# Performance work log

Hardware: AMD Instinct MI355X
Metric: run time of the kernel (lower is better)

## Reference

```python
import jax, jax.numpy as jnp
import numpy as np
from jax import ops as jops

N_NODES = 100000
N_EDGES = 1600000
NEG_SLOPE = 0.2
LN_EPS = 1e-5


def setup_inputs() -> dict:
    key = jax.random.key(0)
    ks = jax.random.split(key, 12)
    inp = {
        "x": jax.random.normal(ks[0], (N_NODES, 4), jnp.float32),
        "edge_index": jax.random.randint(ks[1], (2, N_EDGES), 0, N_NODES, jnp.int64 if jax.config.jax_enable_x64 else jnp.int32),
        # layer 1: GATv2Conv(4, 16, heads=4)
        "W1l": jax.random.normal(ks[2], (4, 64), jnp.float32) * 0.5,
        "W1r": jax.random.normal(ks[3], (4, 64), jnp.float32) * 0.5,
        "a1": jax.random.normal(ks[4], (4, 16), jnp.float32) * 0.5,  # [heads, out]
        "b1": jax.random.normal(ks[5], (64,), jnp.float32) * 0.1,
        "g1": jnp.ones((64,), jnp.float32),
        "be1": jnp.zeros((64,), jnp.float32),
        # layer 2: GATv2Conv(64, 32, heads=1)
        "W2l": jax.random.normal(ks[6], (64, 32), jnp.float32) * 0.125,
        "W2r": jax.random.normal(ks[7], (64, 32), jnp.float32) * 0.125,
        "a2": jax.random.normal(ks[8], (1, 32), jnp.float32) * 0.5,
        "b2": jax.random.normal(ks[9], (32,), jnp.float32) * 0.1,
        "g2": jnp.ones((32,), jnp.float32),
        "be2": jnp.zeros((32,), jnp.float32),
    }
    return inp


def _add_self_loops(edge_index, n):
    loop = jnp.arange(n, dtype=edge_index.dtype)
    return jnp.concatenate([edge_index, jnp.stack([loop, loop])], axis=1)


def _gatv2(x, src, dst, Wl, Wr, att, bias, heads, out_ch, n):
    # x: [N, F]; Wl/Wr: [F, heads*out_ch]; att: [heads, out_ch]
    xl = (x @ Wl).reshape(n, heads, out_ch)  # source transform
    xr = (x @ Wr).reshape(n, heads, out_ch)  # target transform
    e = xl[src] + xr[dst]                     # [E, H, C]
    e = jnp.where(e >= 0, e, NEG_SLOPE * e)   # LeakyReLU(0.2)
    logits = jnp.einsum('ehc,hc->eh', e, att)  # [E, H]
    # segment softmax over destination node
    m = jops.segment_max(logits, dst, num_segments=n)  # [N, H]
    ex = jnp.exp(logits - m[dst])
    denom = jops.segment_sum(ex, dst, num_segments=n)  # [N, H]
    alpha = ex / denom[dst]                            # [E, H]
    out = jops.segment_sum(alpha[:, :, None] * xl[src], dst, num_segments=n)  # [N, H, C]
    return out.reshape(n, heads * out_ch) + bias


def _layernorm(x, g, b):
    mu = jnp.mean(x, axis=-1, keepdims=True)
    var = jnp.mean(jnp.square(x - mu), axis=-1, keepdims=True)
    return (x - mu) * jax.lax.rsqrt(var + LN_EPS) * g + b


def reference(x, edge_index, W1l, W1r, a1, b1, g1, be1, W2l, W2r, a2, b2, g2, be2):
    n = x.shape[0]
    ei = _add_self_loops(edge_index, n)
    src, dst = ei[0], ei[1]
    h = _gatv2(x, src, dst, W1l, W1r, a1, b1, heads=4, out_ch=16, n=n)
    h = _layernorm(h, g1, be1)
    h = jnp.where(h > 0, h, jnp.expm1(h))  # ELU
    h = _gatv2(h, src, dst, W2l, W2r, a2, b2, heads=1, out_ch=32, n=n)
    h = _layernorm(h, g2, be2)
    return h
```

## Files before the change

### kernel.cpp

```cpp
#include <hip/hip_runtime.h>
#include <math.h>

#define NN 100000
#define E0 1600000
#define ETOT (E0 + NN)
#define NEG 0.2f

#define NB 512
#define BS 196
#define CHUNK 4096
#define PPT 16
#define MAXP 4096

__device__ __forceinline__ float leaky(float v) { return fmaxf(v, NEG * v); }

__global__ void k_bhist(const int* __restrict__ ei, int* __restrict__ bcnt) {
    __shared__ int h[NB];
    int tid = threadIdx.x;
    for (int i = tid; i < NB; i += 256) h[i] = 0;
    __syncthreads();
    int stride = gridDim.x * 256;
    for (int e = blockIdx.x * 256 + tid; e < E0; e += stride)
        atomicAdd(&h[ei[E0 + e] / BS], 1);
    __syncthreads();
    for (int i = tid; i < NB; i += 256)
        if (h[i]) atomicAdd(&bcnt[i], h[i]);
}

__global__ void k_bscan(const int* __restrict__ bcnt, int* __restrict__ boff,
                        int* __restrict__ srcsBase, int* __restrict__ cursor) {
    __shared__ int s[NB];
    int tid = threadIdx.x;
    int v = bcnt[tid];
    s[tid] = v;
    __syncthreads();
    for (int off = 1; off < NB; off <<= 1) {
        int t = (tid >= off) ? s[tid - off] : 0;
        __syncthreads();
        s[tid] += t;
        __syncthreads();
    }
    int excl = s[tid] - v;
    boff[tid] = excl;
    cursor[tid] = excl;
    int n0 = tid * BS;
    if (n0 > NN) n0 = NN;
    srcsBase[tid] = excl + n0;
}

__global__ void k_bin(const int* __restrict__ ei, int* __restrict__ cursor,
                      int2* __restrict__ binned) {
    __shared__ int hist[NB];
    __shared__ int basesh[NB];
    int tid = threadIdx.x;
    long long cbase = (long long)blockIdx.x * CHUNK;
    for (int i = tid; i < NB; i += 256) hist[i] = 0;
    __syncthreads();
    int srcv[PPT], dstv[PPT], rank[PPT], bkt[PPT];
#pragma unroll
    for (int k = 0; k < PPT; ++k) {
        long long e = cbase + k * 256 + tid;
        if (e < E0) {
            int s_ = ei[e];
            int d_ = ei[E0 + e];
            int b = d_ / BS;
            rank[k] = atomicAdd(&hist[b], 1);
            srcv[k] = s_;
            dstv[k] = d_;
            bkt[k] = b;
        } else {
            bkt[k] = -1;
        }
    }
    __syncthreads();
    for (int i = tid; i < NB; i += 256)
        if (hist[i] > 0) basesh[i] = atomicAdd(&cursor[i], hist[i]);
    __syncthreads();
#pragma unroll
    for (int k = 0; k < PPT; ++k)
        if (bkt[k] >= 0) {
            int2 p;
            p.x = srcv[k];
            p.y = dstv[k];
            binned[basesh[bkt[k]] + rank[k]] = p;
        }
}

__global__ void k_bfin(const int2* __restrict__ binned, const int* __restrict__ bcnt,
                       const int* __restrict__ boff, const int* __restrict__ srcsBase,
                       int* __restrict__ rs, int* __restrict__ srcs) {
    int b = blockIdx.x;
    int n0 = b * BS;
    if (n0 >= NN) return;
    int nd = NN - n0;
    if (nd > BS) nd = BS;
    int cnt = bcnt[b];
    if (cnt > MAXP) cnt = MAXP;
    int base = boff[b];
    int sb = srcsBase[b];
    __shared__ int ldsCnt[256];
    __shared__ int scanA[256];
    __shared__ int rowOffE[256];
    __shared__ int stage[MAXP + BS];
    int tid = threadIdx.x;
    ldsCnt[tid] = 0;
    __syncthreads();
    int srcv[PPT], dl_[PPT], rk_[PPT];
#pragma unroll
    for (int k = 0; k < PPT; ++k) {
        int i = k * 256 + tid;
        if (i < cnt) {
            int2 p = binned[base + i];
            int dl = p.y - n0;
            rk_[k] = atomicAdd(&ldsCnt[dl], 1);
            srcv[k] = p.x;
            dl_[k] = dl;
        } else {
            dl_[k] = -1;
        }
    }
    __syncthreads();
    int v = (tid < nd) ? ldsCnt[tid] + 1 : 0;
    scanA[tid] = v;
    __syncthreads();
    for (int off = 1; off < 256; off <<= 1) {
        int t = (tid >= off) ? scanA[tid - off] : 0;
        __syncthreads();
        scanA[tid] += t;
        __syncthreads();
    }
    rowOffE[tid] = scanA[tid] - v;
    __syncthreads();
    if (tid < nd) {
        int e = rowOffE[tid];
        rs[n0 + tid] = sb + e;
        stage[e] = n0 + tid;
    }
    __syncthreads();
#pragma unroll
    for (int k = 0; k < PPT; ++k)
        if (dl_[k] >= 0) stage[rowOffE[dl_[k]] + 1 + rk_[k]] = srcv[k];
    __syncthreads();
    int tot = cnt + nd;
    for (int i = tid; i < tot; i += 256) srcs[sb + i] = stage[i];
}

__global__ void k_gat1(const float* __restrict__ x, const float* __restrict__ Wl,
                       const float* __restrict__ Wr, const float* __restrict__ att,
                       const int* __restrict__ rs, const int* __restrict__ srcs,
                       const float* __restrict__ b, const float* __restrict__ g,
                       const float* __restrict__ be, float* __restrict__ h) {
    int lane = threadIdx.x & 63;
    int wave = (blockIdx.x * blockDim.x + threadIdx.x) >> 6;
    int nwaves = (gridDim.x * blockDim.x) >> 6;
    int e_i = lane >> 3;
    int sub = lane & 7;
    float wl[4][8], wr[4][8], at[8];
#pragma unroll
    for (int k = 0; k < 4; ++k)
#pragma unroll
        for (int j = 0; j < 8; ++j) {
            wl[k][j] = Wl[k * 64 + sub * 8 + j];
            wr[k][j] = Wr[k * 64 + sub * 8 + j];
        }
#pragma unroll
    for (int j = 0; j < 8; ++j) at[j] = att[sub * 8 + j];

    for (int n = wave; n < NN; n += nwaves) {
        const float4 xd = *(const float4*)(x + (long long)n * 4);
        float xrd[8];
#pragma unroll
        for (int j = 0; j < 8; ++j)
            xrd[j] = xd.x * wr[0][j] + xd.y * wr[1][j] + xd.z * wr[2][j] +
                     xd.w * wr[3][j];
        int beg = rs[n];
        int end = (n == NN - 1) ? ETOT : rs[n + 1];
        float acc[8] = {0.f, 0.f, 0.f, 0.f, 0.f, 0.f, 0.f, 0.f};
        float den = 0.f;
        for (int base = beg; base < end; base += 8) {
            int slot = base + e_i;
            bool valid = slot < end;
            int s = srcs[valid ? slot : beg];
            const float4 xa = *(const float4*)(x + (long long)s * 4);
            float xls[8];
            float p = 0.f;
#pragma unroll
            for (int j = 0; j < 8; ++j) {
                float t = xa.x * wl[0][j] + xa.y * wl[1][j] + xa.z * wl[2][j] +
                          xa.w * wl[3][j];
                xls[j] = t;
                float u = t + xrd[j];
                u = fmaxf(u, NEG * u);
                p += u * at[j];
            }
            p += __shfl_xor(p, 1);
            float ex = valid ? __expf(p) : 0.f;
            den += ex;
#pragma unroll
            for (int j = 0; j < 8; ++j) acc[j] += ex * xls[j];
        }
#pragma unroll
        for (int m = 8; m <= 32; m <<= 1) {
#pragma unroll
            for (int j = 0; j < 8; ++j) acc[j] += __shfl_xor(acc[j], m);
            den += __shfl_xor(den, m);
        }
        float v = acc[0];
#pragma unroll
        for (int j = 1; j < 8; ++j) v = (e_i == j) ? acc[j] : v;
        int cf = sub * 8 + e_i;
        v = v / den + b[cf];
        float s1 = v;
#pragma unroll
        for (int m = 1; m < 64; m <<= 1) s1 += __shfl_xor(s1, m);
        float mu = s1 * (1.f / 64.f);
        float c = v - mu;
        float sq = c * c;
#pragma unroll
        for (int m = 1; m < 64; m <<= 1) sq += __shfl_xor(sq, m);
        float y = c * rsqrtf(sq * (1.f / 64.f) + 1e-5f) * g[cf] + be[cf];
        h[(long long)n * 64 + cf] = y > 0.f ? y : expm1f(y);
    }
}

__global__ void k_lin2(const float* __restrict__ h, const float* __restrict__ Wl,
                       const float* __restrict__ Wr, float* __restrict__ xl2,
                       float* __restrict__ xr2) {
    __shared__ float wl_s[2048];
    __shared__ float wr_s[2048];
    for (int i = threadIdx.x; i < 2048; i += blockDim.x) {
        wl_s[i] = Wl[i];
        wr_s[i] = Wr[i];
    }
    __syncthreads();
    int t = blockIdx.x * blockDim.x + threadIdx.x;
    if (t >= NN * 32) return;
    int n = t >> 5, j = t & 31;
    const float* hr = h + (long long)n * 64;
    float al = 0.f, ar = 0.f;
#pragma unroll 8
    for (int k = 0; k < 64; ++k) {
        float hv = hr[k];
        al += hv * wl_s[k * 32 + j];
        ar += hv * wr_s[k * 32 + j];
    }
    xl2[(long long)n * 32 + j] = al;
    xr2[(long long)n * 32 + j] = ar;
}

__global__ void k_gat2(const float* __restrict__ xl2, const float* __restrict__ xr2,
                       const float* __restrict__ att, const int* __restrict__ rs,
                       const int* __restrict__ srcs, const float* __restrict__ b,
                       const float* __restrict__ g, const float* __restrict__ be,
                       float* __restrict__ out) {
    int lane = threadIdx.x & 63;
    int wave = (blockIdx.x * blockDim.x + threadIdx.x) >> 6;
    int nwaves = (gridDim.x * blockDim.x) >> 6;
    int e_i = lane >> 3;
    int cg = lane & 7;
    float at[4];
#pragma unroll
    for (int j = 0; j < 4; ++j) at[j] = att[cg * 4 + j];

    for (int n = wave; n < NN; n += nwaves) {
        const float4 xr4 = *(const float4*)(xr2 + (long long)n * 32 + cg * 4);
        float xrd[4] = {xr4.x, xr4.y, xr4.z, xr4.w};
        int beg = rs[n];
        int end = (n == NN - 1) ? ETOT : rs[n + 1];
        float acc[4] = {0.f, 0.f, 0.f, 0.f};
        float den = 0.f;
        for (int base = beg; base < end; base += 8) {
            int slot = base + e_i;
            bool valid = slot < end;
            int s = srcs[valid ? slot : beg];
            const float4 xa = *(const float4*)(xl2 + (long long)s * 32 + cg * 4);
            float xls[4] = {xa.x, xa.y, xa.z, xa.w};
            float p = 0.f;
#pragma unroll
            for (int j = 0; j < 4; ++j) {
                float u = xls[j] + xrd[j];
                u = fmaxf(u, NEG * u);
                p += u * at[j];
            }
            p += __shfl_xor(p, 1);
            p += __shfl_xor(p, 2);
            p += __shfl_xor(p, 4);
            float ex = valid ? __expf(p) : 0.f;
            den += ex;
#pragma unroll
            for (int j = 0; j < 4; ++j) acc[j] += ex * xls[j];
        }
#pragma unroll
        for (int m = 8; m <= 32; m <<= 1) {
#pragma unroll
            for (int j = 0; j < 4; ++j) acc[j] += __shfl_xor(acc[j], m);
            den += __shfl_xor(den, m);
        }
        int e3 = e_i & 3;
        float v = acc[0];
#pragma unroll
        for (int j = 1; j < 4; ++j) v = (e3 == j) ? acc[j] : v;
        int cf = cg * 4 + e3;
        v = v / den + b[cf];
        float s1 = v;
#pragma unroll
        for (int m = 1; m < 64; m <<= 1) s1 += __shfl_xor(s1, m);
        float mu = s1 * (1.f / 64.f);
        float cc = v - mu;
        float sq = cc * cc;
#pragma unroll
        for (int m = 1; m < 64; m <<= 1) sq += __shfl_xor(sq, m);
        float y = cc * rsqrtf(sq * (1.f / 64.f) + 1e-5f) * g[cf] + be[cf];
        if (e_i < 4) out[(long long)n * 32 + cf] = y;
    }
}

extern "C" void kernel_launch(void* const* d_in, const int* in_sizes, int n_in,
                              void* d_out, int out_size, void* d_ws, size_t ws_size,
                              hipStream_t stream) {
    const float* x   = (const float*)d_in[0];
    const int*   ei  = (const int*)d_in[1];
    const float* W1l = (const float*)d_in[2];
    const float* W1r = (const float*)d_in[3];
    const float* a1  = (const float*)d_in[4];
    const float* b1  = (const float*)d_in[5];
    const float* g1  = (const float*)d_in[6];
    const float* be1 = (const float*)d_in[7];
    const float* W2l = (const float*)d_in[8];
    const float* W2r = (const float*)d_in[9];
    const float* a2  = (const float*)d_in[10];
    const float* b2  = (const float*)d_in[11];
    const float* g2  = (const float*)d_in[12];
    const float* be2 = (const float*)d_in[13];
    float* out = (float*)d_out;

    float* ws = (float*)d_ws;
    float* h   = ws;
    float* xl2 = ws + 6400000;
    float* xr2 = ws + 9600000;
    int2* binned = (int2*)ws;
    int* ib        = (int*)(ws + 12800000);
    int* rs        = ib;
    int* srcs      = ib + 100000;
    int* bcnt      = ib + 1800000;
    int* boff      = ib + 1800000 + NB;
    int* srcsBase  = ib + 1800000 + 2 * NB;
    int* cursor    = ib + 1800000 + 3 * NB;

    hipMemsetAsync(bcnt, 0, NB * sizeof(int), stream);
    k_bhist<<<256, 256, 0, stream>>>(ei, bcnt);
    k_bscan<<<1, NB, 0, stream>>>(bcnt, boff, srcsBase, cursor);
    k_bin<<<(E0 + CHUNK - 1) / CHUNK, 256, 0, stream>>>(ei, cursor, binned);
    k_bfin<<<NB, 256, 0, stream>>>(binned, bcnt, boff, srcsBase, rs, srcs);

    k_gat1<<<1024, 256, 0, stream>>>(x, W1l, W1r, a1, rs, srcs, b1, g1, be1, h);
    k_lin2<<<(NN * 32 + 255) / 256, 256, 0, stream>>>(h, W2l, W2r, xl2, xr2);
    k_gat2<<<2048, 256, 0, stream>>>(xl2, xr2, a2, rs, srcs, b2, g2, be2, out);
}
```

Measured before the change: 228.7 us.

## Aggregate raw features in GAT layer 1, precompute target transform, prefetch next edge

Layer 1 now accumulates the attention-weighted raw 4-dim source features and applies Wl once per node after aggregation, instead of accumulating all 8 transformed channels per edge. The target projection moves to a new k_linr kernel that writes xr1 to the workspace, so k_gat1 no longer computes it per node. Both GAT kernels software-prefetch the next edge's source index and features, and gain launch bounds plus a larger grid for layer 1. The cost is an extra kernel launch and the 25.6MB xr1 write and read, which reuses the region later overwritten by xl2.

```diff
diff --git a/kernel.cpp b/kernel.cpp
--- a/kernel.cpp
+++ b/kernel.cpp
@@ -145,50 +145,65 @@
     for (int i = tid; i < tot; i += 256) srcs[sb + i] = stage[i];
 }
 
-__global__ void k_gat1(const float* __restrict__ x, const float* __restrict__ Wl,
-                       const float* __restrict__ Wr, const float* __restrict__ att,
-                       const int* __restrict__ rs, const int* __restrict__ srcs,
-                       const float* __restrict__ b, const float* __restrict__ g,
-                       const float* __restrict__ be, float* __restrict__ h) {
+__global__ void k_linr(const float* __restrict__ x, const float* __restrict__ Wr,
+                       float* __restrict__ xr1) {
+    int t = blockIdx.x * blockDim.x + threadIdx.x;
+    if (t >= NN * 16) return;
+    int n = t >> 4;
+    int j = (t & 15) << 2;
+    const float4 xv = *(const float4*)(x + (long long)n * 4);
+    float4 a = {0.f, 0.f, 0.f, 0.f};
+#pragma unroll
+    for (int k = 0; k < 4; ++k) {
+        float4 w = *(const float4*)(Wr + k * 64 + j);
+        float xk = k == 0 ? xv.x : k == 1 ? xv.y : k == 2 ? xv.z : xv.w;
+        a.x += xk * w.x; a.y += xk * w.y;
+        a.z += xk * w.z; a.w += xk * w.w;
+    }
+    *(float4*)(xr1 + (long long)n * 64 + j) = a;
+}
+
+__global__ __launch_bounds__(256, 8) void k_gat1(
+        const float* __restrict__ x, const float* __restrict__ Wl,
+        const float* __restrict__ xr1, const float* __restrict__ att,
+        const int* __restrict__ rs, const int* __restrict__ srcs,
+        const float* __restrict__ b, const float* __restrict__ g,
+        const float* __restrict__ be, float* __restrict__ h) {
     int lane = threadIdx.x & 63;
     int wave = (blockIdx.x * blockDim.x + threadIdx.x) >> 6;
     int nwaves = (gridDim.x * blockDim.x) >> 6;
     int e_i = lane >> 3;
     int sub = lane & 7;
-    float wl[4][8], wr[4][8], at[8];
+    float wl[4][8], at[8];
 #pragma unroll
     for (int k = 0; k < 4; ++k)
 #pragma unroll
-        for (int j = 0; j < 8; ++j) {
-            wl[k][j] = Wl[k * 64 + sub * 8 + j];
-            wr[k][j] = Wr[k * 64 + sub * 8 + j];
-        }
+        for (int j = 0; j < 8; ++j) wl[k][j] = Wl[k * 64 + sub * 8 + j];
 #pragma unroll
     for (int j = 0; j < 8; ++j) at[j] = att[sub * 8 + j];
 
     for (int n = wave; n < NN; n += nwaves) {
-        const float4 xd = *(const float4*)(x + (long long)n * 4);
-        float xrd[8];
-#pragma unroll
-        for (int j = 0; j < 8; ++j)
-            xrd[j] = xd.x * wr[0][j] + xd.y * wr[1][j] + xd.z * wr[2][j] +
-                     xd.w * wr[3][j];
+        const float4 r0 = *(const float4*)(xr1 + (long long)n * 64 + sub * 8);
+        const float4 r1 = *(const float4*)(xr1 + (long long)n * 64 + sub * 8 + 4);
+        float xrd[8] = {r0.x, r0.y, r0.z, r0.w, r1.x, r1.y, r1.z, r1.w};
         int beg = rs[n];
         int end = (n == NN - 1) ? ETOT : rs[n + 1];
-        float acc[8] = {0.f, 0.f, 0.f, 0.f, 0.f, 0.f, 0.f, 0.f};
+        float acc4[4] = {0.f, 0.f, 0.f, 0.f};
         float den = 0.f;
+        int slot = beg + e_i;
+        bool valid = slot < end;
+        int s = srcs[valid ? slot : beg];
+        float4 xa = *(const float4*)(x + (long long)s * 4);
         for (int base = beg; base < end; base += 8) {
-            int slot = base + e_i;
-            bool valid = slot < end;
-            int s = srcs[valid ? slot : beg];
-            const float4 xa = *(const float4*)(x + (long long)s * 4);
-            float xls[8];
+            int nslot = base + 8 + e_i;
+            bool nvalid = nslot < end;
+            int ns = srcs[nvalid ? nslot : beg];
+            float4 xn = *(const float4*)(x + (long long)ns * 4);
             float p = 0.f;
 #pragma unroll
             for (int j = 0; j < 8; ++j) {
                 float t = xa.x * wl[0][j] + xa.y * wl[1][j] + xa.z * wl[2][j] +
                           xa.w * wl[3][j];
-                xls[j] = t;
                 float u = t + xrd[j];
                 u = fmaxf(u, NEG * u);
                 p += u * at[j];
@@ -196,20 +211,22 @@
             p += __shfl_xor(p, 1);
             float ex = valid ? __expf(p) : 0.f;
             den += ex;
-#pragma unroll
-            for (int j = 0; j < 8; ++j) acc[j] += ex * xls[j];
+            acc4[0] += ex * xa.x;
+            acc4[1] += ex * xa.y;
+            acc4[2] += ex * xa.z;
+            acc4[3] += ex * xa.w;
+            xa = xn;
+            valid = nvalid;
         }
 #pragma unroll
         for (int m = 8; m <= 32; m <<= 1) {
 #pragma unroll
-            for (int j = 0; j < 8; ++j) acc[j] += __shfl_xor(acc[j], m);
+            for (int k = 0; k < 4; ++k) acc4[k] += __shfl_xor(acc4[k], m);
             den += __shfl_xor(den, m);
         }
-        float v = acc[0];
-#pragma unroll
-        for (int j = 1; j < 8; ++j) v = (e_i == j) ? acc[j] : v;
         int cf = sub * 8 + e_i;
-        v = v / den + b[cf];
+        float v = (acc4[0] * Wl[cf] + acc4[1] * Wl[64 + cf] +
+                   acc4[2] * Wl[128 + cf] + acc4[3] * Wl[192 + cf]) / den + b[cf];
         float s1 = v;
 #pragma unroll
         for (int m = 1; m < 64; m <<= 1) s1 += __shfl_xor(s1, m);
@@ -248,11 +265,12 @@
     xr2[(long long)n * 32 + j] = ar;
 }
 
-__global__ void k_gat2(const float* __restrict__ xl2, const float* __restrict__ xr2,
-                       const float* __restrict__ att, const int* __restrict__ rs,
-                       const int* __restrict__ srcs, const float* __restrict__ b,
-                       const float* __restrict__ g, const float* __restrict__ be,
-                       float* __restrict__ out) {
+__global__ __launch_bounds__(256, 8) void k_gat2(
+        const float* __restrict__ xl2, const float* __restrict__ xr2,
+        const float* __restrict__ att, const int* __restrict__ rs,
+        const int* __restrict__ srcs, const float* __restrict__ b,
+        const float* __restrict__ g, const float* __restrict__ be,
+        float* __restrict__ out) {
     int lane = threadIdx.x & 63;
     int wave = (blockIdx.x * blockDim.x + threadIdx.x) >> 6;
     int nwaves = (gridDim.x * blockDim.x) >> 6;
@@ -269,16 +287,20 @@
         int end = (n == NN - 1) ? ETOT : rs[n + 1];
         float acc[4] = {0.f, 0.f, 0.f, 0.f};
         float den = 0.f;
+        int slot = beg + e_i;
+        bool valid = slot < end;
+        int s = srcs[valid ? slot : beg];
+        float4 xa = *(const float4*)(xl2 + (long long)s * 32 + cg * 4);
         for (int base = beg; base < end; base += 8) {
-            int slot = base + e_i;
-            bool valid = slot < end;
-            int s = srcs[valid ? slot : beg];
-            const float4 xa = *(const float4*)(xl2 + (long long)s * 32 + cg * 4);
-            float xls[4] = {xa.x, xa.y, xa.z, xa.w};
+            int nslot = base + 8 + e_i;
+            bool nvalid = nslot < end;
+            int ns = srcs[nvalid ? nslot : beg];
+            float4 xn = *(const float4*)(xl2 + (long long)ns * 32 + cg * 4);
             float p = 0.f;
 #pragma unroll
             for (int j = 0; j < 4; ++j) {
-                float u = xls[j] + xrd[j];
+                float xls = j == 0 ? xa.x : j == 1 ? xa.y : j == 2 ? xa.z : xa.w;
+                float u = xls + xrd[j];
                 u = fmaxf(u, NEG * u);
                 p += u * at[j];
             }
@@ -287,8 +309,12 @@
             p += __shfl_xor(p, 4);
             float ex = valid ? __expf(p) : 0.f;
             den += ex;
-#pragma unroll
-            for (int j = 0; j < 4; ++j) acc[j] += ex * xls[j];
+            acc[0] += ex * xa.x;
+            acc[1] += ex * xa.y;
+            acc[2] += ex * xa.z;
+            acc[3] += ex * xa.w;
+            xa = xn;
+            valid = nvalid;
         }
 #pragma unroll
         for (int m = 8; m <= 32; m <<= 1) {
@@ -336,6 +362,7 @@
 
     float* ws = (float*)d_ws;
     float* h   = ws;
+    float* xr1 = ws + 6400000;
     float* xl2 = ws + 6400000;
     float* xr2 = ws + 9600000;
     int2* binned = (int2*)ws;
@@ -352,8 +379,9 @@
     k_bscan<<<1, NB, 0, stream>>>(bcnt, boff, srcsBase, cursor);
     k_bin<<<(E0 + CHUNK - 1) / CHUNK, 256, 0, stream>>>(ei, cursor, binned);
     k_bfin<<<NB, 256, 0, stream>>>(binned, bcnt, boff, srcsBase, rs, srcs);
-
-    k_gat1<<<1024, 256, 0, stream>>>(x, W1l, W1r, a1, rs, srcs, b1, g1, be1, h);
+    k_linr<<<(NN * 16 + 255) / 256, 256, 0, stream>>>(x, W1r, xr1);
+
+    k_gat1<<<2048, 256, 0, stream>>>(x, W1l, xr1, a1, rs, srcs, b1, g1, be1, h);
     k_lin2<<<(NN * 32 + 255) / 256, 256, 0, stream>>>(h, W2l, W2r, xl2, xr2);
     k_gat2<<<2048, 256, 0, stream>>>(xl2, xr2, a2, rs, srcs, b2, g2, be2, out);
 }
```

New measurement: 344.5 us. 50.7% more time.
